# Kernel tuning notes

Hardware: AMD Instinct MI355X
Metric: run time of the kernel (lower is better)

## Reference

```python
import jax, jax.numpy as jnp
import numpy as np

B, R, T, C = 32, 256, 512, 16
C1, C2 = 64, 128


def setup_inputs() -> dict:
    key = jax.random.key(0)
    ks = jax.random.split(key, 9)
    s = 0.05
    return {
        "x": jax.random.normal(ks[0], (B, R, T, C), dtype=jnp.float32),
        "W_edge": jax.random.normal(ks[1], (C1, C, R), dtype=jnp.float32) * s,
        "b_edge": jax.random.normal(ks[2], (C1,), dtype=jnp.float32) * s,
        "W1": jax.random.normal(ks[3], (R // 4, R), dtype=jnp.float32) * s,
        "b1": jax.random.normal(ks[4], (R // 4,), dtype=jnp.float32) * s,
        "W2": jax.random.normal(ks[5], (R, R // 4), dtype=jnp.float32) * s,
        "b2": jax.random.normal(ks[6], (R,), dtype=jnp.float32) * s,
        "W_node": jax.random.normal(ks[7], (C2, C1, R), dtype=jnp.float32) * s,
        "b_node": jax.random.normal(ks[8], (C2,), dtype=jnp.float32) * s,
    }


def reference(x, W_edge, b_edge, W1, b1, W2, b2, W_node, b_node):
    # ---- Pearson correlation: x [B,R,T,C] -> pcc [B,C,R,R] ----
    xp = jnp.transpose(x, (0, 3, 1, 2))            # [B,C,R,T]
    xc = xp - jnp.mean(xp, axis=-1, keepdims=True)  # centered
    cov = jnp.einsum('bcrt,bcit->bcri', xc, xc)     # [B,C,R,R]
    norm = jnp.sqrt(jnp.sum(xc * xc, axis=-1))      # [B,C,R]
    pcc = cov / (norm[:, :, :, None] * norm[:, :, None, :])
    # ---- EdgeConv: Conv2d(C,C1,kernel=(1,R)) -> [B,R,C1] (width collapsed) ----
    e = jnp.einsum('bcrk,ock->bro', pcc, W_edge) + b_edge  # [B,R,C1]
    e = jax.nn.leaky_relu(e, negative_slope=0.01)
    # ---- FC_SAtt: avgpool over C1, MLP over rois, sigmoid ----
    pooled = jnp.mean(e, axis=-1)                   # [B,R]
    h = jax.nn.relu(pooled @ W1.T + b1)             # [B,R//4]
    att = jax.nn.sigmoid(h @ W2.T + b2)             # [B,R]
    # ---- attention-weighted aggregation (q=k=1 in the einsum) ----
    out = att[:, :, None] * e                       # [B,R,C1]
    # ---- NodeConv: Conv2d(C1,C2,kernel=(R,1)) -> [B,C2] ----
    o = jnp.einsum('brc,ocr->bo', out, W_node) + b_node
    o = jax.nn.leaky_relu(o, negative_slope=0.01)
    return o[:, None, None, :], att[:, :, None, None]  # [B,1,1,C2], [B,R,1,1]
```

## Files before the change

### kernel.cpp

```cpp
#include <hip/hip_runtime.h>
#include <hip/hip_bf16.h>

#define B_  32
#define R_  256
#define T_  512
#define C_  16
#define C1_ 64
#define C2_ 128

typedef short short8 __attribute__((ext_vector_type(8)));
typedef float f32x4  __attribute__((ext_vector_type(4)));

__device__ __forceinline__ unsigned short f2bf(float f) {
    unsigned u = __float_as_uint(f);
    return (unsigned short)((u + 0x7fffu + ((u >> 16) & 1u)) >> 16);
}

__global__ __launch_bounds__(256) void k0_wcvt(const float* __restrict__ W,
                                               unsigned short* __restrict__ Wb) {
    const int i = (blockIdx.x * 256 + threadIdx.x) * 4;
    float4 v = *(const float4*)(W + i);
    uint2 pk;
    pk.x = (unsigned)f2bf(v.x) | ((unsigned)f2bf(v.y) << 16);
    pk.y = (unsigned)f2bf(v.z) | ((unsigned)f2bf(v.w) << 16);
    *(uint2*)(Wb + i) = pk;
}

__global__ __launch_bounds__(256) void k1_normalize(const float* __restrict__ x,
                                                    unsigned short* __restrict__ y) {
    const int r = blockIdx.x, b = blockIdx.y, tid = threadIdx.x;
    __shared__ float xs[T_ * C_];
    __shared__ float psum[16][17], psq[16][17];
    __shared__ float s_mean[16], s_inv[16];

    const float4* src = reinterpret_cast<const float4*>(x + ((size_t)(b * R_ + r)) * T_ * C_);
    float4* dst = reinterpret_cast<float4*>(xs);
#pragma unroll
    for (int j = 0; j < 8; ++j) dst[tid + j * 256] = src[tid + j * 256];
    __syncthreads();

    {
        const int c = tid & 15, seg = tid >> 4;
        float s = 0.f, q = 0.f;
#pragma unroll
        for (int i = 0; i < 32; ++i) {
            float v = xs[(seg * 32 + i) * C_ + c];
            s += v; q += v * v;
        }
        psum[seg][c] = s; psq[seg][c] = q;
    }
    __syncthreads();
    if (tid < 16) {
        float S = 0.f, Q = 0.f;
#pragma unroll
        for (int g = 0; g < 16; ++g) { S += psum[g][tid]; Q += psq[g][tid]; }
        float mean = S * (1.f / T_);
        float nrm2 = Q - S * mean;
        s_mean[tid] = mean;
        s_inv[tid] = rsqrtf(nrm2);
    }
    __syncthreads();

    const int cc = tid >> 4, l = tid & 15;
    const float mean = s_mean[cc], inv = s_inv[cc];
    unsigned* out = reinterpret_cast<unsigned*>(y + (((size_t)(b * C_ + cc)) * R_ + r) * T_);
#pragma unroll
    for (int j = 0; j < 16; ++j) {
        const int t = j * 32 + l * 2;
        float v0 = (xs[t * C_ + cc] - mean) * inv;
        float v1 = (xs[(t + 1) * C_ + cc] - mean) * inv;
        out[t >> 1] = (unsigned)f2bf(v0) | ((unsigned)f2bf(v1) << 16);
    }
}

__global__ __launch_bounds__(256) void k1t_transpose(const unsigned short* __restrict__ y,
                                                     unsigned short* __restrict__ yT) {
    const int c = blockIdx.x, b = blockIdx.y;
    const unsigned short* src = y + ((size_t)(b * C_ + c)) * R_ * T_;
    unsigned short* dstp = yT + ((size_t)(b * C_ + c)) * T_ * R_;
    const int tg = threadIdx.x & 7;
    const int r0 = (threadIdx.x >> 3) * 8;
#pragma unroll 4
    for (int it = 0; it < 16; ++it) {
        const int t0 = (tg + 8 * it) * 4;
        uint2 u[8];
#pragma unroll
        for (int k = 0; k < 8; ++k)
            u[k] = *(const uint2*)(src + (size_t)(r0 + k) * T_ + t0);
#pragma unroll
        for (int j = 0; j < 4; ++j) {
            unsigned e[8];
#pragma unroll
            for (int k = 0; k < 8; ++k) {
                unsigned comp = (j < 2) ? u[k].x : u[k].y;
                e[k] = (j & 1) ? (comp >> 16) : (comp & 0xffffu);
            }
            uint4 o4;
            o4.x = e[0] | (e[1] << 16);
            o4.y = e[2] | (e[3] << 16);
            o4.z = e[4] | (e[5] << 16);
            o4.w = e[6] | (e[7] << 16);
            *(uint4*)(dstp + (size_t)(t0 + j) * R_ + r0) = o4;
        }
    }
}

__global__ __launch_bounds__(256) void k2_mfma(const unsigned short* __restrict__ yT,
                                               const unsigned short* __restrict__ Wb,
                                               unsigned short* __restrict__ Z) {
    const int th = blockIdx.x, c = blockIdx.y, b = blockIdx.z;
    const int tid = threadIdx.x;
    const int w = tid >> 6, l = tid & 63;
    const int lm = l & 15, lk = (l >> 4) * 8;

    const unsigned short* ab = yT + ((size_t)(b * C_ + c)) * T_ * R_;
    const unsigned short* wb = Wb + (size_t)c * R_;
    const int tbase = th * 256 + w * 64;

    f32x4 acc[4][4];
#pragma unroll
    for (int i = 0; i < 4; ++i)
#pragma unroll
        for (int j = 0; j < 4; ++j) acc[i][j] = (f32x4){0.f, 0.f, 0.f, 0.f};

    for (int r0 = 0; r0 < R_; r0 += 32) {
        short8 A[4], Bf[4];
#pragma unroll
        for (int mt = 0; mt < 4; ++mt)
            A[mt] = *(const short8*)(ab + (size_t)(tbase + mt * 16 + lm) * R_ + r0 + lk);
#pragma unroll
        for (int nt = 0; nt < 4; ++nt)
            Bf[nt] = *(const short8*)(wb + (size_t)(nt * 16 + lm) * (C_ * R_) + r0 + lk);
#pragma unroll
        for (int mt = 0; mt < 4; ++mt)
#pragma unroll
            for (int nt = 0; nt < 4; ++nt)
                acc[mt][nt] = __builtin_amdgcn_mfma_f32_16x16x32_bf16(A[mt], Bf[nt], acc[mt][nt], 0, 0, 0);
    }

    const int rowb = (l >> 4) * 4;
#pragma unroll
    for (int mt = 0; mt < 4; ++mt) {
#pragma unroll
        for (int nt = 0; nt < 4; ++nt) {
            const int o = nt * 16 + lm;
            const int tb = tbase + mt * 16 + rowb;
            uint2 pk;
            pk.x = (unsigned)f2bf(acc[mt][nt][0]) | ((unsigned)f2bf(acc[mt][nt][1]) << 16);
            pk.y = (unsigned)f2bf(acc[mt][nt][2]) | ((unsigned)f2bf(acc[mt][nt][3]) << 16);
            *(uint2*)(Z + (((size_t)b * C1_ + o) * C_ + c) * T_ + tb) = pk;
        }
    }
}

__global__ __launch_bounds__(256) void k3_mfma(const unsigned short* __restrict__ y,
                                               const unsigned short* __restrict__ Z,
                                               float* __restrict__ partial) {
    const int c = blockIdx.x, b = blockIdx.y;
    const int tid = threadIdx.x;
    const int w = tid >> 6, l = tid & 63;
    const int lm = l & 15, lk = (l >> 4) * 8;

    const unsigned short* yb = y + ((size_t)(b * C_ + c)) * R_ * T_;
    const unsigned short* zb = Z + ((size_t)b * C1_ * C_ + c) * T_;

    f32x4 acc[4][4];
#pragma unroll
    for (int i = 0; i < 4; ++i)
#pragma unroll
        for (int j = 0; j < 4; ++j) acc[i][j] = (f32x4){0.f, 0.f, 0.f, 0.f};

    for (int t0 = 0; t0 < T_; t0 += 32) {
        short8 A[4], Bf[4];
#pragma unroll
        for (int mt = 0; mt < 4; ++mt)
            A[mt] = *(const short8*)(yb + (size_t)(w * 64 + mt * 16 + lm) * T_ + t0 + lk);
#pragma unroll
        for (int nt = 0; nt < 4; ++nt)
            Bf[nt] = *(const short8*)(zb + (size_t)(nt * 16 + lm) * (C_ * T_) + t0 + lk);
#pragma unroll
        for (int mt = 0; mt < 4; ++mt)
#pragma unroll
            for (int nt = 0; nt < 4; ++nt)
                acc[mt][nt] = __builtin_amdgcn_mfma_f32_16x16x32_bf16(A[mt], Bf[nt], acc[mt][nt], 0, 0, 0);
    }

    const int rowb = (l >> 4) * 4;
#pragma unroll
    for (int mt = 0; mt < 4; ++mt) {
#pragma unroll
        for (int nt = 0; nt < 4; ++nt) {
            const int o = nt * 16 + lm;
            const int rb = w * 64 + mt * 16 + rowb;
            float* d = partial + (((size_t)c * B_ + b) * C1_ + o) * R_ + rb;
            *(float4*)d = make_float4(acc[mt][nt][0], acc[mt][nt][1], acc[mt][nt][2], acc[mt][nt][3]);
        }
    }
}

__global__ __launch_bounds__(256) void k3b_combine(const float* __restrict__ partial,
                                                   const float* __restrict__ b_edge,
                                                   float* __restrict__ eT) {
    const int idx4 = blockIdx.x * 256 + threadIdx.x;
    const float4* p = (const float4*)partial;
    float4 s = p[idx4];
#pragma unroll
    for (int c = 1; c < C_; ++c) {
        float4 v = p[(size_t)c * 131072 + idx4];
        s.x += v.x; s.y += v.y; s.z += v.z; s.w += v.w;
    }
    const float bo = b_edge[(idx4 >> 6) & 63];
    s.x += bo; s.y += bo; s.z += bo; s.w += bo;
    s.x = s.x >= 0.f ? s.x : 0.01f * s.x;
    s.y = s.y >= 0.f ? s.y : 0.01f * s.y;
    s.z = s.z >= 0.f ? s.z : 0.01f * s.z;
    s.w = s.w >= 0.f ? s.w : 0.01f * s.w;
    ((float4*)eT)[idx4] = s;
}

__global__ __launch_bounds__(256) void k4_att(const float* __restrict__ eT,
                                              const float* __restrict__ W1, const float* __restrict__ b1,
                                              const float* __restrict__ W2, const float* __restrict__ b2,
                                              float* __restrict__ out_att) {
    const int b = blockIdx.x, tid = threadIdx.x;
    __shared__ float pooled[R_];
    __shared__ float h[64];
    {
        const float* eb = eT + (size_t)b * C1_ * R_;
        float s = 0.f;
#pragma unroll
        for (int o = 0; o < C1_; ++o) s += eb[o * R_ + tid];
        pooled[tid] = s * (1.f / 64.f);
    }
    __syncthreads();
    if (tid < 64) {
        float a = b1[tid];
        const float* w = W1 + tid * R_;
        for (int r = 0; r < R_; ++r) a += w[r] * pooled[r];
        h[tid] = fmaxf(a, 0.f);
    }
    __syncthreads();
    {
        float a = b2[tid];
        const float* w = W2 + tid * 64;
#pragma unroll
        for (int j = 0; j < 64; ++j) a += w[j] * h[j];
        out_att[b * R_ + tid] = 1.f / (1.f + __expf(-a));
    }
}

__global__ __launch_bounds__(256) void k5_gemm(const float* __restrict__ eT,
                                               const float* __restrict__ att,
                                               const float* __restrict__ W_node,
                                               float* __restrict__ partial) {
    const int kc = blockIdx.x;
    const int k0 = kc * 64;
    const int r0 = k0 & 255;
    const int tid = threadIdx.x;

    __shared__ __align__(16) float gs[32 * 68];
    __shared__ __align__(16) float Ws[128 * 68];
    float4* gs4 = reinterpret_cast<float4*>(gs);
    float4* Ws4 = reinterpret_cast<float4*>(Ws);

    {
        const int b = tid >> 3;
        const float4* ebase = reinterpret_cast<const float4*>(eT) + (size_t)b * 4096 + (k0 >> 2);
        const float4* abase = reinterpret_cast<const float4*>(att + b * R_ + r0);
#pragma unroll
        for (int j = 0; j < 2; ++j) {
            const int kk4 = (tid & 7) + j * 8;
            float4 v = ebase[kk4];
            float4 a = abase[kk4];
            v.x *= a.x; v.y *= a.y; v.z *= a.z; v.w *= a.w;
            gs4[b * 17 + kk4] = v;
        }
    }
    {
        const float4* wbase = reinterpret_cast<const float4*>(W_node) + (k0 >> 2);
#pragma unroll
        for (int j = 0; j < 8; ++j) {
            const int i = j * 256 + tid;
            const int oc = i >> 4, col4 = i & 15;
            Ws4[oc * 17 + col4] = wbase[(size_t)oc * 4096 + col4];
        }
    }
    __syncthreads();

    const int tx = tid & 31, ty = tid >> 5;
    float acc[4][4];
#pragma unroll
    for (int i = 0; i < 4; ++i)
#pragma unroll
        for (int j = 0; j < 4; ++j) acc[i][j] = 0.f;

#pragma unroll
    for (int kk4 = 0; kk4 < 16; ++kk4) {
        float4 g4[4], w4[4];
#pragma unroll
        for (int i = 0; i < 4; ++i) g4[i] = gs4[(ty + 8 * i) * 17 + kk4];
#pragma unroll
        for (int j = 0; j < 4; ++j) w4[j] = Ws4[(tx + 32 * j) * 17 + kk4];
#pragma unroll
        for (int i = 0; i < 4; ++i)
#pragma unroll
            for (int j = 0; j < 4; ++j)
                acc[i][j] += g4[i].x * w4[j].x + g4[i].y * w4[j].y
                           + g4[i].z * w4[j].z + g4[i].w * w4[j].w;
    }

    float* d = partial + (size_t)kc * (B_ * C2_);
#pragma unroll
    for (int i = 0; i < 4; ++i)
#pragma unroll
        for (int j = 0; j < 4; ++j)
            d[(ty + 8 * i) * C2_ + tx + 32 * j] = acc[i][j];
}

__global__ __launch_bounds__(256) void k5_reduce(const float* __restrict__ partial,
                                                 const float* __restrict__ b_node,
                                                 float* __restrict__ out_o) {
    const int idx = blockIdx.x * 256 + threadIdx.x;
    float s = 0.f;
    for (int kc = 0; kc < 256; ++kc) s += partial[(size_t)kc * (B_ * C2_) + idx];
    s += b_node[idx & 127];
    out_o[idx] = s >= 0.f ? s : 0.01f * s;
}

extern "C" void kernel_launch(void* const* d_in, const int* in_sizes, int n_in,
                              void* d_out, int out_size, void* d_ws, size_t ws_size,
                              hipStream_t stream) {
    const float* x      = (const float*)d_in[0];
    const float* W_edge = (const float*)d_in[1];
    const float* b_edge = (const float*)d_in[2];
    const float* W1     = (const float*)d_in[3];
    const float* b1     = (const float*)d_in[4];
    const float* W2     = (const float*)d_in[5];
    const float* b2     = (const float*)d_in[6];
    const float* W_node = (const float*)d_in[7];
    const float* b_node = (const float*)d_in[8];
    float* out = (float*)d_out;

    char* ws = (char*)d_ws;
    unsigned short* y  = (unsigned short*)ws;
    unsigned short* yT = (unsigned short*)(ws + 134217728);
    float* partial3    = (float*)(ws + 134217728);
    unsigned short* Z  = (unsigned short*)(ws + 268435456);
    unsigned short* Wb = (unsigned short*)(ws + 301989888);
    float* eT          = (float*)(ws + 302514176);
    float* partial5    = (float*)(ws + 304611328);

    k0_wcvt<<<256, 256, 0, stream>>>(W_edge, Wb);
    k1_normalize<<<dim3(R_, B_), 256, 0, stream>>>(x, y);
    k1t_transpose<<<dim3(C_, B_), 256, 0, stream>>>(y, yT);
    k2_mfma<<<dim3(2, C_, B_), 256, 0, stream>>>(yT, Wb, Z);
    k3_mfma<<<dim3(C_, B_), 256, 0, stream>>>(y, Z, partial3);
    k3b_combine<<<512, 256, 0, stream>>>(partial3, b_edge, eT);
    k4_att<<<B_, 256, 0, stream>>>(eT, W1, b1, W2, b2, out + 4096);
    k5_gemm<<<256, 256, 0, stream>>>(eT, out + 4096, W_node, partial5);
    k5_reduce<<<16, 256, 0, stream>>>(partial5, b_node, out);
}
```

Before: 570.8 us.

## Fuse channel reduction into k3 MFMA kernel and parallelize attention MLP

Replaces the per-channel k3 GEMM that wrote 16 partial fp32 slices to global memory, and the separate combine kernel, with one kernel. It tiles over ROI blocks, with each wave handling 4 channels, and reduces across waves in LDS before applying bias and leaky-ReLU. This removes a large partial-sum write and read round trip and one launch. The cost is less register-level reuse of Z fragments, since each wave now loads 4 B fragments per A fragment, and repeated Z reads across ROI-tile blocks. The attention MLP's first layer is also split across all 256 threads instead of 64.

Result: slower. 597.8 us (+4.7%).

```diff
diff --git a/kernel.cpp b/kernel.cpp
--- a/kernel.cpp
+++ b/kernel.cpp
@@ -153,69 +153,67 @@
     }
 }
 
-__global__ __launch_bounds__(256) void k3_mfma(const unsigned short* __restrict__ y,
-                                               const unsigned short* __restrict__ Z,
-                                               float* __restrict__ partial) {
-    const int c = blockIdx.x, b = blockIdx.y;
+__global__ __launch_bounds__(256) void k3_fused(const unsigned short* __restrict__ y,
+                                                const unsigned short* __restrict__ Z,
+                                                const float* __restrict__ b_edge,
+                                                float* __restrict__ eT) {
+    const int bid = blockIdx.x;
+    const int b = bid & 31, rt = bid >> 5;
+    const int r0 = rt * 16;
     const int tid = threadIdx.x;
     const int w = tid >> 6, l = tid & 63;
     const int lm = l & 15, lk = (l >> 4) * 8;
 
-    const unsigned short* yb = y + ((size_t)(b * C_ + c)) * R_ * T_;
-    const unsigned short* zb = Z + ((size_t)b * C1_ * C_ + c) * T_;
-
-    f32x4 acc[4][4];
-#pragma unroll
-    for (int i = 0; i < 4; ++i)
-#pragma unroll
-        for (int j = 0; j < 4; ++j) acc[i][j] = (f32x4){0.f, 0.f, 0.f, 0.f};
-
-    for (int t0 = 0; t0 < T_; t0 += 32) {
-        short8 A[4], Bf[4];
-#pragma unroll
-        for (int mt = 0; mt < 4; ++mt)
-            A[mt] = *(const short8*)(yb + (size_t)(w * 64 + mt * 16 + lm) * T_ + t0 + lk);
-#pragma unroll
-        for (int nt = 0; nt < 4; ++nt)
-            Bf[nt] = *(const short8*)(zb + (size_t)(nt * 16 + lm) * (C_ * T_) + t0 + lk);
-#pragma unroll
-        for (int mt = 0; mt < 4; ++mt)
-#pragma unroll
-            for (int nt = 0; nt < 4; ++nt)
-                acc[mt][nt] = __builtin_amdgcn_mfma_f32_16x16x32_bf16(A[mt], Bf[nt], acc[mt][nt], 0, 0, 0);
+    __shared__ float red[4][C1_ * 17];
+
+    f32x4 acc[4];
+#pragma unroll
+    for (int j = 0; j < 4; ++j) acc[j] = (f32x4){0.f, 0.f, 0.f, 0.f};
+
+    const unsigned short* yb = y + (size_t)b * C_ * R_ * T_;
+    const unsigned short* zb = Z + (size_t)b * C1_ * C_ * T_;
+
+#pragma unroll
+    for (int cc = 0; cc < 4; ++cc) {
+        const int c = w * 4 + cc;
+        const unsigned short* ya = yb + ((size_t)c * R_ + r0 + lm) * T_ + lk;
+        const unsigned short* za = zb + ((size_t)(lm * C_ + c)) * T_ + lk;
+#pragma unroll 4
+        for (int t0 = 0; t0 < T_; t0 += 32) {
+            short8 A  = *(const short8*)(ya + t0);
+            short8 B0 = *(const short8*)(za + t0);
+            short8 B1 = *(const short8*)(za + (size_t)16 * C_ * T_ + t0);
+            short8 B2 = *(const short8*)(za + (size_t)32 * C_ * T_ + t0);
+            short8 B3 = *(const short8*)(za + (size_t)48 * C_ * T_ + t0);
+            acc[0] = __builtin_amdgcn_mfma_f32_16x16x32_bf16(A, B0, acc[0], 0, 0, 0);
+            acc[1] = __builtin_amdgcn_mfma_f32_16x16x32_bf16(A, B1, acc[1], 0, 0, 0);
+            acc[2] = __builtin_amdgcn_mfma_f32_16x16x32_bf16(A, B2, acc[2], 0, 0, 0);
+            acc[3] = __builtin_amdgcn_mfma_f32_16x16x32_bf16(A, B3, acc[3], 0, 0, 0);
+        }
     }
 
     const int rowb = (l >> 4) * 4;
 #pragma unroll
-    for (int mt = 0; mt < 4; ++mt) {
-#pragma unroll
-        for (int nt = 0; nt < 4; ++nt) {
-            const int o = nt * 16 + lm;
-            const int rb = w * 64 + mt * 16 + rowb;
-            float* d = partial + (((size_t)c * B_ + b) * C1_ + o) * R_ + rb;
-            *(float4*)d = make_float4(acc[mt][nt][0], acc[mt][nt][1], acc[mt][nt][2], acc[mt][nt][3]);
-        }
-    }
-}
-
-__global__ __launch_bounds__(256) void k3b_combine(const float* __restrict__ partial,
-                                                   const float* __restrict__ b_edge,
-                                                   float* __restrict__ eT) {
-    const int idx4 = blockIdx.x * 256 + threadIdx.x;
-    const float4* p = (const float4*)partial;
-    float4 s = p[idx4];
-#pragma unroll
-    for (int c = 1; c < C_; ++c) {
-        float4 v = p[(size_t)c * 131072 + idx4];
-        s.x += v.x; s.y += v.y; s.z += v.z; s.w += v.w;
-    }
-    const float bo = b_edge[(idx4 >> 6) & 63];
-    s.x += bo; s.y += bo; s.z += bo; s.w += bo;
-    s.x = s.x >= 0.f ? s.x : 0.01f * s.x;
-    s.y = s.y >= 0.f ? s.y : 0.01f * s.y;
-    s.z = s.z >= 0.f ? s.z : 0.01f * s.z;
-    s.w = s.w >= 0.f ? s.w : 0.01f * s.w;
-    ((float4*)eT)[idx4] = s;
+    for (int nt = 0; nt < 4; ++nt) {
+        const int o = nt * 16 + lm;
+#pragma unroll
+        for (int j = 0; j < 4; ++j)
+            red[w][o * 17 + rowb + j] = acc[nt][j];
+    }
+    __syncthreads();
+
+    {
+        const int r = tid & 15, og = tid >> 4;
+#pragma unroll
+        for (int k = 0; k < 4; ++k) {
+            const int o = og * 4 + k;
+            const int a = o * 17 + r;
+            float s = red[0][a] + red[1][a] + red[2][a] + red[3][a];
+            s += b_edge[o];
+            s = s >= 0.f ? s : 0.01f * s;
+            eT[((size_t)b * C1_ + o) * R_ + r0 + r] = s;
+        }
+    }
 }
 
 __global__ __launch_bounds__(256) void k4_att(const float* __restrict__ eT,
@@ -224,6 +222,7 @@
                                               float* __restrict__ out_att) {
     const int b = blockIdx.x, tid = threadIdx.x;
     __shared__ float pooled[R_];
+    __shared__ float hp[4][64];
     __shared__ float h[64];
     {
         const float* eb = eT + (size_t)b * C1_ * R_;
@@ -233,12 +232,18 @@
         pooled[tid] = s * (1.f / 64.f);
     }
     __syncthreads();
-    if (tid < 64) {
-        float a = b1[tid];
-        const float* w = W1 + tid * R_;
-        for (int r = 0; r < R_; ++r) a += w[r] * pooled[r];
-        h[tid] = fmaxf(a, 0.f);
-    }
+    {
+        const int i = tid & 63, q = tid >> 6;
+        const float* w = W1 + i * R_ + q * 64;
+        const float* p = pooled + q * 64;
+        float a = 0.f;
+#pragma unroll
+        for (int r = 0; r < 64; ++r) a += w[r] * p[r];
+        hp[q][i] = a;
+    }
+    __syncthreads();
+    if (tid < 64)
+        h[tid] = fmaxf(b1[tid] + hp[0][tid] + hp[1][tid] + hp[2][tid] + hp[3][tid], 0.f);
     __syncthreads();
     {
         float a = b2[tid];
@@ -344,7 +349,6 @@
     char* ws = (char*)d_ws;
     unsigned short* y  = (unsigned short*)ws;
     unsigned short* yT = (unsigned short*)(ws + 134217728);
-    float* partial3    = (float*)(ws + 134217728);
     unsigned short* Z  = (unsigned short*)(ws + 268435456);
     unsigned short* Wb = (unsigned short*)(ws + 301989888);
     float* eT          = (float*)(ws + 302514176);
@@ -354,8 +358,7 @@
     k1_normalize<<<dim3(R_, B_), 256, 0, stream>>>(x, y);
     k1t_transpose<<<dim3(C_, B_), 256, 0, stream>>>(y, yT);
     k2_mfma<<<dim3(2, C_, B_), 256, 0, stream>>>(yT, Wb, Z);
-    k3_mfma<<<dim3(C_, B_), 256, 0, stream>>>(y, Z, partial3);
-    k3b_combine<<<512, 256, 0, stream>>>(partial3, b_edge, eT);
+    k3_fused<<<512, 256, 0, stream>>>(y, Z, b_edge, eT);
     k4_att<<<B_, 256, 0, stream>>>(eT, W1, b1, W2, b2, out + 4096);
     k5_gemm<<<256, 256, 0, stream>>>(eT, out + 4096, W_node, partial5);
     k5_reduce<<<16, 256, 0, stream>>>(partial5, b_node, out);
```

## Fuse y transpose into k2 MFMA via double-buffered LDS tiles

Applied to the files above, without the earlier changes.

Removes the standalone transpose kernel that wrote a full transposed bf16 copy of y (128 MB) to global memory. k2 now loads y tiles directly, transposes them in registers into a padded, double-buffered LDS buffer, and prefetches the next 32-row chunk while MFMAs run on the current one. The workspace layout is compacted to match. Separately, the attention MLP's first layer is split across all 256 threads with partial sums reduced in shared memory, instead of running on 64 threads only. The fused version adds a barrier per K-step and LDS traffic to k2.

Measured after the change: 504.3 us. 11.7% less time.

```diff
diff --git a/kernel.cpp b/kernel.cpp
--- a/kernel.cpp
+++ b/kernel.cpp
@@ -73,20 +73,34 @@
     }
 }
 
-__global__ __launch_bounds__(256) void k1t_transpose(const unsigned short* __restrict__ y,
-                                                     unsigned short* __restrict__ yT) {
-    const int c = blockIdx.x, b = blockIdx.y;
-    const unsigned short* src = y + ((size_t)(b * C_ + c)) * R_ * T_;
-    unsigned short* dstp = yT + ((size_t)(b * C_ + c)) * T_ * R_;
-    const int tg = threadIdx.x & 7;
-    const int r0 = (threadIdx.x >> 3) * 8;
-#pragma unroll 4
-    for (int it = 0; it < 16; ++it) {
-        const int t0 = (tg + 8 * it) * 4;
+__global__ __launch_bounds__(256) void k2_mfma(const unsigned short* __restrict__ y,
+                                               const unsigned short* __restrict__ Wb,
+                                               unsigned short* __restrict__ Z) {
+    const int th = blockIdx.x, c = blockIdx.y, b = blockIdx.z;
+    const int tid = threadIdx.x;
+    const int w = tid >> 6, l = tid & 63;
+    const int lm = l & 15, lk = (l >> 4) * 8;
+
+    __shared__ __align__(16) unsigned short ldsT[2][256 * 40];
+
+    const unsigned short* yb = y + ((size_t)(b * C_ + c)) * R_ * T_;
+    const unsigned short* wb = Wb + (size_t)c * R_;
+    const int tb0 = th * 256;
+
+    const int st_t0 = (tid & 63) * 4;
+    const int st_r0 = (tid >> 6) * 8;
+
+    f32x4 acc[4][4];
+#pragma unroll
+    for (int i = 0; i < 4; ++i)
+#pragma unroll
+        for (int j = 0; j < 4; ++j) acc[i][j] = (f32x4){0.f, 0.f, 0.f, 0.f};
+
+    {
+        const unsigned short* src = yb + (size_t)st_r0 * T_ + tb0 + st_t0;
         uint2 u[8];
 #pragma unroll
-        for (int k = 0; k < 8; ++k)
-            u[k] = *(const uint2*)(src + (size_t)(r0 + k) * T_ + t0);
+        for (int k = 0; k < 8; ++k) u[k] = *(const uint2*)(src + (size_t)k * T_);
 #pragma unroll
         for (int j = 0; j < 4; ++j) {
             unsigned e[8];
@@ -100,34 +114,25 @@
             o4.y = e[2] | (e[3] << 16);
             o4.z = e[4] | (e[5] << 16);
             o4.w = e[6] | (e[7] << 16);
-            *(uint4*)(dstp + (size_t)(t0 + j) * R_ + r0) = o4;
-        }
-    }
-}
-
-__global__ __launch_bounds__(256) void k2_mfma(const unsigned short* __restrict__ yT,
-                                               const unsigned short* __restrict__ Wb,
-                                               unsigned short* __restrict__ Z) {
-    const int th = blockIdx.x, c = blockIdx.y, b = blockIdx.z;
-    const int tid = threadIdx.x;
-    const int w = tid >> 6, l = tid & 63;
-    const int lm = l & 15, lk = (l >> 4) * 8;
-
-    const unsigned short* ab = yT + ((size_t)(b * C_ + c)) * T_ * R_;
-    const unsigned short* wb = Wb + (size_t)c * R_;
-    const int tbase = th * 256 + w * 64;
-
-    f32x4 acc[4][4];
-#pragma unroll
-    for (int i = 0; i < 4; ++i)
-#pragma unroll
-        for (int j = 0; j < 4; ++j) acc[i][j] = (f32x4){0.f, 0.f, 0.f, 0.f};
-
-    for (int r0 = 0; r0 < R_; r0 += 32) {
+            *(uint4*)&ldsT[0][(st_t0 + j) * 40 + st_r0] = o4;
+        }
+    }
+    __syncthreads();
+
+    for (int s = 0; s < 8; ++s) {
+        const int r0 = s * 32;
+        uint2 u[8];
+        if (s < 7) {
+            const unsigned short* src = yb + (size_t)(r0 + 32 + st_r0) * T_ + tb0 + st_t0;
+#pragma unroll
+            for (int k = 0; k < 8; ++k) u[k] = *(const uint2*)(src + (size_t)k * T_);
+        }
+
+        const unsigned short* base = &ldsT[s & 1][0];
         short8 A[4], Bf[4];
 #pragma unroll
         for (int mt = 0; mt < 4; ++mt)
-            A[mt] = *(const short8*)(ab + (size_t)(tbase + mt * 16 + lm) * R_ + r0 + lk);
+            A[mt] = *(const short8*)(base + (w * 64 + mt * 16 + lm) * 40 + lk);
 #pragma unroll
         for (int nt = 0; nt < 4; ++nt)
             Bf[nt] = *(const short8*)(wb + (size_t)(nt * 16 + lm) * (C_ * R_) + r0 + lk);
@@ -136,9 +141,30 @@
 #pragma unroll
             for (int nt = 0; nt < 4; ++nt)
                 acc[mt][nt] = __builtin_amdgcn_mfma_f32_16x16x32_bf16(A[mt], Bf[nt], acc[mt][nt], 0, 0, 0);
+
+        if (s < 7) {
+            unsigned short* nbuf = &ldsT[(s + 1) & 1][0];
+#pragma unroll
+            for (int j = 0; j < 4; ++j) {
+                unsigned e[8];
+#pragma unroll
+                for (int k = 0; k < 8; ++k) {
+                    unsigned comp = (j < 2) ? u[k].x : u[k].y;
+                    e[k] = (j & 1) ? (comp >> 16) : (comp & 0xffffu);
+                }
+                uint4 o4;
+                o4.x = e[0] | (e[1] << 16);
+                o4.y = e[2] | (e[3] << 16);
+                o4.z = e[4] | (e[5] << 16);
+                o4.w = e[6] | (e[7] << 16);
+                *(uint4*)&nbuf[(st_t0 + j) * 40 + st_r0] = o4;
+            }
+        }
+        __syncthreads();
     }
 
     const int rowb = (l >> 4) * 4;
+    const int tbase = tb0 + w * 64;
 #pragma unroll
     for (int mt = 0; mt < 4; ++mt) {
 #pragma unroll
@@ -224,6 +250,7 @@
                                               float* __restrict__ out_att) {
     const int b = blockIdx.x, tid = threadIdx.x;
     __shared__ float pooled[R_];
+    __shared__ float hp[4][64];
     __shared__ float h[64];
     {
         const float* eb = eT + (size_t)b * C1_ * R_;
@@ -233,12 +260,18 @@
         pooled[tid] = s * (1.f / 64.f);
     }
     __syncthreads();
-    if (tid < 64) {
-        float a = b1[tid];
-        const float* w = W1 + tid * R_;
-        for (int r = 0; r < R_; ++r) a += w[r] * pooled[r];
-        h[tid] = fmaxf(a, 0.f);
-    }
+    {
+        const int i = tid & 63, q = tid >> 6;
+        const float* w = W1 + i * R_ + q * 64;
+        const float* p = pooled + q * 64;
+        float a = 0.f;
+#pragma unroll
+        for (int r = 0; r < 64; ++r) a += w[r] * p[r];
+        hp[q][i] = a;
+    }
+    __syncthreads();
+    if (tid < 64)
+        h[tid] = fmaxf(b1[tid] + hp[0][tid] + hp[1][tid] + hp[2][tid] + hp[3][tid], 0.f);
     __syncthreads();
     {
         float a = b2[tid];
@@ -343,17 +376,15 @@
 
     char* ws = (char*)d_ws;
     unsigned short* y  = (unsigned short*)ws;
-    unsigned short* yT = (unsigned short*)(ws + 134217728);
-    float* partial3    = (float*)(ws + 134217728);
-    unsigned short* Z  = (unsigned short*)(ws + 268435456);
-    unsigned short* Wb = (unsigned short*)(ws + 301989888);
-    float* eT          = (float*)(ws + 302514176);
-    float* partial5    = (float*)(ws + 304611328);
+    unsigned short* Z  = (unsigned short*)(ws + 134217728);
+    unsigned short* Wb = (unsigned short*)(ws + 167772160);
+    float* partial3    = (float*)(ws + 168296448);
+    float* eT          = (float*)(ws + 201850880);
+    float* partial5    = (float*)(ws + 203948032);
 
     k0_wcvt<<<256, 256, 0, stream>>>(W_edge, Wb);
     k1_normalize<<<dim3(R_, B_), 256, 0, stream>>>(x, y);
-    k1t_transpose<<<dim3(C_, B_), 256, 0, stream>>>(y, yT);
-    k2_mfma<<<dim3(2, C_, B_), 256, 0, stream>>>(yT, Wb, Z);
+    k2_mfma<<<dim3(2, C_, B_), 256, 0, stream>>>(y, Wb, Z);
     k3_mfma<<<dim3(C_, B_), 256, 0, stream>>>(y, Z, partial3);
     k3b_combine<<<512, 256, 0, stream>>>(partial3, b_edge, eT);
     k4_att<<<B_, 256, 0, stream>>>(eT, W1, b1, W2, b2, out + 4096);
```
